# Performance work log

Measured on AMD Instinct MI355X. Metric: run time of the kernel, lower is better.

The kernel has to match this reference:

```python
import jax, jax.numpy as jnp
import numpy as np
from jax import lax

L, H, DH, D, FF = 8, 16, 64, 1024, 4096  # layers, heads, head dim, model dim, mlp hidden
B, S = 4, 512
EPS = 1e-5


def setup_inputs() -> dict:
    key = jax.random.key(0)
    ks = jax.random.split(key, 8)
    std = 0.02
    return {
        "x": jax.random.normal(ks[0], (B, S, D), jnp.float32),
        "ln1_w": jnp.ones((L, D), jnp.float32),
        "ln1_b": jnp.zeros((L, D), jnp.float32),
        "qw": jax.random.normal(ks[1], (L, H, DH, DH), jnp.float32) * std,
        "qb": jnp.zeros((L, H, DH), jnp.float32),
        "kw": jax.random.normal(ks[2], (L, H, DH, DH), jnp.float32) * std,
        "kb": jnp.zeros((L, H, DH), jnp.float32),
        "vw": jax.random.normal(ks[3], (L, H, DH, DH), jnp.float32) * std,
        "vb": jnp.zeros((L, H, DH), jnp.float32),
        "ln2_w": jnp.ones((L, D), jnp.float32),
        "ln2_b": jnp.zeros((L, D), jnp.float32),
        "w1": jax.random.normal(ks[4], (L, D, FF), jnp.float32) * std,
        "b1": jnp.zeros((L, FF), jnp.float32),
        "w2": jax.random.normal(ks[5], (L, FF, D), jnp.float32) * std,
        "b2": jnp.zeros((L, D), jnp.float32),
    }


def _layernorm(x, w, b):
    m = jnp.mean(x, axis=-1, keepdims=True)
    v = jnp.mean(jnp.square(x - m), axis=-1, keepdims=True)
    return (x - m) * lax.rsqrt(v + EPS) * w + b


def reference(x, ln1_w, ln1_b, qw, qb, kw, kb, vw, vb, ln2_w, ln2_b, w1, b1, w2, b2):
    b, s, d = x.shape
    scale = 1.0 / jnp.sqrt(jnp.asarray(DH, x.dtype))

    def layer(h, p):
        (l1w, l1b, Qw, Qb, Kw, Kb, Vw, Vb, l2w, l2b, W1, B1, W2, B2) = p
        y = _layernorm(h, l1w, l1b)
        yh = y.reshape(b, s, H, DH)
        # nn.Linear per head: y @ W.T + b, W is [out=e, in=d]
        q = jnp.einsum('bshd,hed->bshe', yh, Qw) + Qb
        k = jnp.einsum('bshd,hed->bshe', yh, Kw) + Kb
        v = jnp.einsum('bshd,hed->bshe', yh, Vw) + Vb
        attn = jax.nn.softmax(jnp.einsum('bshe,bthe->bhst', q, k) * scale, axis=-1)
        o = jnp.einsum('bhst,bthe->bshe', attn, v).reshape(b, s, d)
        h = h + o
        z = _layernorm(h, l2w, l2b)
        z = jax.nn.gelu(z @ W1 + B1, approximate=False) @ W2 + B2
        return h + z, None

    params = (ln1_w, ln1_b, qw, qb, kw, kb, vw, vb, ln2_w, ln2_b, w1, b1, w2, b2)
    out, _ = lax.scan(layer, x, params)
    return out
```

## Files before the change

kernel.cpp:

```cpp
#include <hip/hip_runtime.h>
#include <hip/hip_bf16.h>

typedef __hip_bfloat16 bf16;
typedef __bf16 bf16x8 __attribute__((ext_vector_type(8)));
typedef float f32x4 __attribute__((ext_vector_type(4)));
typedef unsigned short u16;
typedef unsigned int u32;

#define SEQ 512
#define DMODEL 1024
#define FFDIM 4096
#define NHEAD 16
#define HDIM 64
#define NB 4
#define NLAYER 8

__device__ __forceinline__ u16 f2bu(float f) {
    union { bf16 h; u16 u; } c; c.h = __float2bfloat16(f); return c.u;
}

__device__ __forceinline__ void gload16(const bf16* g, bf16* l) {
    __builtin_amdgcn_global_load_lds(
        (const __attribute__((address_space(1))) unsigned int*)g,
        (__attribute__((address_space(3))) unsigned int*)l,
        16, 0, 0);
}

template<int BM, int BN, int BK, int WM, int WN>
__device__ __forceinline__ void gemm_core(
    const bf16* __restrict__ A, int lda,
    const bf16* __restrict__ B, int ldb,
    int K,
    f32x4 (&acc)[WM/16][WN/16],
    bf16* lA, bf16* lB)
{
    constexpr int NFM = WM / 16, NFN = WN / 16;
    constexpr int WC = BN / WN;
    const int tid  = threadIdx.x;
    const int lane = tid & 63, wave = tid >> 6;
    const int wr = wave / WC, wc = wave % WC;
    const int l15 = lane & 15, l4 = lane >> 4;

    constexpr int ITA = (BM * BK) / (256 * 8);
    constexpr int ITB = (BN * BK) / (256 * 8);

    for (int kt = 0; kt < K; kt += BK) {
        __syncthreads();
#pragma unroll
        for (int it = 0; it < ITA; ++it) {
            const int f = (it * 256 + tid) * 8;
            const int r = f / BK, c = f % BK;
            gload16(A + (long)r * lda + kt + c, lA + f);
        }
#pragma unroll
        for (int it = 0; it < ITB; ++it) {
            const int f = (it * 256 + tid) * 8;
            const int r = f / BK, c = f % BK;
            gload16(B + (long)r * ldb + kt + c, lB + f);
        }
        __syncthreads();
#pragma unroll
        for (int ks = 0; ks < BK / 32; ++ks) {
            bf16x8 af[NFM], bfr[NFN];
#pragma unroll
            for (int fm = 0; fm < NFM; ++fm)
                af[fm] = *(const bf16x8*)(lA + (wr * WM + fm * 16 + l15) * BK + ks * 32 + l4 * 8);
#pragma unroll
            for (int fn = 0; fn < NFN; ++fn)
                bfr[fn] = *(const bf16x8*)(lB + (wc * WN + fn * 16 + l15) * BK + ks * 32 + l4 * 8);
#pragma unroll
            for (int fm = 0; fm < NFM; ++fm)
#pragma unroll
                for (int fn = 0; fn < NFN; ++fn)
                    acc[fm][fn] = __builtin_amdgcn_mfma_f32_16x16x32_bf16(
                        af[fm], bfr[fn], acc[fm][fn], 0, 0, 0);
        }
    }
}

__global__ __launch_bounds__(256) void k_ln(const float* __restrict__ h,
                                            const float* __restrict__ w,
                                            const float* __restrict__ bp,
                                            bf16* __restrict__ out)
{
    const int row = blockIdx.x;
    const int tid = threadIdx.x;
    const float4 x = ((const float4*)(h + (long)row * DMODEL))[tid];
    float s  = x.x + x.y + x.z + x.w;
    float s2 = x.x * x.x + x.y * x.y + x.z * x.z + x.w * x.w;
#pragma unroll
    for (int off = 32; off; off >>= 1) { s += __shfl_xor(s, off); s2 += __shfl_xor(s2, off); }
    __shared__ float rs[4], rs2[4];
    const int wave = tid >> 6;
    if ((tid & 63) == 0) { rs[wave] = s; rs2[wave] = s2; }
    __syncthreads();
    const float S1 = rs[0] + rs[1] + rs[2] + rs[3];
    const float S2 = rs2[0] + rs2[1] + rs2[2] + rs2[3];
    const float mean = S1 * (1.0f / DMODEL);
    const float var  = S2 * (1.0f / DMODEL) - mean * mean;
    const float rstd = rsqrtf(var + 1e-5f);
    const float4 wv = ((const float4*)w)[tid];
    const float4 bv = ((const float4*)bp)[tid];
    uint2 o;
    o.x = (u32)f2bu((x.x - mean) * rstd * wv.x + bv.x) |
          ((u32)f2bu((x.y - mean) * rstd * wv.y + bv.y) << 16);
    o.y = (u32)f2bu((x.z - mean) * rstd * wv.z + bv.z) |
          ((u32)f2bu((x.w - mean) * rstd * wv.w + bv.w) << 16);
    ((uint2*)(out + (long)row * DMODEL))[tid] = o;
}

__global__ __launch_bounds__(256) void k_transw(const float* __restrict__ w1,
                                                const float* __restrict__ w2,
                                                bf16* __restrict__ w1t,
                                                bf16* __restrict__ w2t)
{
    __shared__ float t[64][65];
    int bid = blockIdx.x;
    const float* src; bf16* dst; int R, C, rb, cb;
    if (bid < 1024) {
        src = w1; dst = w1t; R = DMODEL; C = FFDIM;
        rb = (bid >> 6) << 6; cb = (bid & 63) << 6;
    } else {
        bid -= 1024;
        src = w2; dst = w2t; R = FFDIM; C = DMODEL;
        rb = (bid >> 4) << 6; cb = (bid & 15) << 6;
    }
    const int tid = threadIdx.x;
#pragma unroll
    for (int i = 0; i < 16; ++i) {
        int flat = i * 256 + tid;
        int r = flat >> 6, c = flat & 63;
        t[r][c] = src[(long)(rb + r) * C + cb + c];
    }
    __syncthreads();
#pragma unroll
    for (int i = 0; i < 16; ++i) {
        int flat = i * 256 + tid;
        int c = flat >> 6, r = flat & 63;
        dst[(long)(cb + c) * R + rb + r] = __float2bfloat16(t[r][c]);
    }
}

__global__ __launch_bounds__(256) void k_qkv2(const bf16* __restrict__ y,
                                              const float* __restrict__ qwl,
                                              const float* __restrict__ kwl,
                                              const float* __restrict__ vwl,
                                              const float* __restrict__ qb,
                                              const float* __restrict__ kb,
                                              const float* __restrict__ vb,
                                              bf16* __restrict__ qh,
                                              bf16* __restrict__ kh,
                                              bf16* __restrict__ vt)
{
    __shared__ __align__(16) char lmem[128 * 64 * 2 + 64 * 64 * 2];
    bf16* lA = (bf16*)lmem;
    char* lBb = lmem + 128 * 64 * 2;

    const int tid = threadIdx.x;
    const int lane = tid & 63, wave = tid >> 6;
    const int l15 = lane & 15, l4 = lane >> 4;
    const int z = blockIdx.y;
    const int b = z >> 4, hd = z & 15;
    const bf16* A = y + (long)b * SEQ * DMODEL + hd * HDIM + (long)blockIdx.x * 128 * DMODEL;

#pragma unroll
    for (int it = 0; it < 4; ++it) {
        const int f = (it * 256 + tid) * 8;
        const int r = f >> 6, c = f & 63;
        gload16(A + (long)r * DMODEL + c, lA + f);
    }
    __syncthreads();

    bf16x8 qa[2][2];
#pragma unroll
    for (int fm = 0; fm < 2; ++fm)
#pragma unroll
        for (int ks = 0; ks < 2; ++ks)
            qa[fm][ks] = *(const bf16x8*)(lA + (wave * 32 + fm * 16 + l15) * 64 + ks * 32 + l4 * 8);

    for (int t = 0; t < 3; ++t) {
        __syncthreads();
        const float* Bsrc = ((t == 0) ? qwl : (t == 1) ? kwl : vwl) + (long)hd * HDIM * HDIM;
#pragma unroll
        for (int it = 0; it < 4; ++it) {
            const int f = (it * 256 + tid) * 4;
            const float4 v = *(const float4*)(Bsrc + f);
            uint2 o;
            o.x = (u32)f2bu(v.x) | ((u32)f2bu(v.y) << 16);
            o.y = (u32)f2bu(v.z) | ((u32)f2bu(v.w) << 16);
            const int row = f >> 6;
            const int byte = (f << 1) ^ ((row & 7) << 4);
            *(uint2*)(lBb + byte) = o;
        }
        __syncthreads();

        bf16x8 bfr[4][2];
#pragma unroll
        for (int fn = 0; fn < 4; ++fn)
#pragma unroll
            for (int ks = 0; ks < 2; ++ks) {
                const int row = fn * 16 + l15;
                int byte = (row << 7) + ((ks * 32 + l4 * 8) << 1);
                byte ^= (row & 7) << 4;
                bfr[fn][ks] = *(const bf16x8*)(lBb + byte);
            }
        f32x4 acc[2][4] = {};
#pragma unroll
        for (int ks = 0; ks < 2; ++ks)
#pragma unroll
            for (int fm = 0; fm < 2; ++fm)
#pragma unroll
                for (int fn = 0; fn < 4; ++fn)
                    acc[fm][fn] = __builtin_amdgcn_mfma_f32_16x16x32_bf16(
                        qa[fm][ks], bfr[fn][ks], acc[fm][fn], 0, 0, 0);

        const float* bias = (t == 0) ? qb : (t == 1) ? kb : vb;
#pragma unroll
        for (int fm = 0; fm < 2; ++fm)
#pragma unroll
            for (int fn = 0; fn < 4; ++fn)
#pragma unroll
                for (int r = 0; r < 4; ++r) {
                    const int srow = blockIdx.x * 128 + wave * 32 + fm * 16 + l4 * 4 + r;
                    const int e = fn * 16 + l15;
                    float v = acc[fm][fn][r] + bias[hd * HDIM + e];
                    if (t == 0) {
                        qh[((long)z * SEQ + srow) * HDIM + e] = __float2bfloat16(v * 0.125f);
                    } else if (t == 1) {
                        kh[((long)z * SEQ + srow) * HDIM + e] = __float2bfloat16(v);
                    } else {
                        vt[((long)z * HDIM + e) * SEQ + srow] = __float2bfloat16(v);
                    }
                }
    }
}

__global__ __launch_bounds__(256) void k_flash(const bf16* __restrict__ qh,
                                               const bf16* __restrict__ kh,
                                               const bf16* __restrict__ vt,
                                               float* __restrict__ h)
{
    __shared__ __align__(16) char lmem[24576];
    bf16* lQ = (bf16*)lmem;
    char* lKb = lmem + 8192;
    char* lVb = lmem + 16384;

    const int tid = threadIdx.x;
    const int lane = tid & 63, wave = tid >> 6;
    const int l15 = lane & 15, l4 = lane >> 4;
    const int z = blockIdx.y;
    const int b = z >> 4, hd = z & 15;
    const int q0 = blockIdx.x * 64;

    const bf16* Qsrc = qh + ((long)z * SEQ + q0) * HDIM;
#pragma unroll
    for (int it = 0; it < 2; ++it) {
        const int f = (it * 256 + tid) * 8;
        gload16(Qsrc + f, lQ + f);
    }
    __syncthreads();

    bf16x8 qa[2];
#pragma unroll
    for (int ks = 0; ks < 2; ++ks)
        qa[ks] = *(const bf16x8*)(lQ + (wave * 16 + l15) * 64 + ks * 32 + l4 * 8);

    char* lPb = lmem + wave * 2048;

    f32x4 O[4] = {};
    float mrun[4], lrun[4];
#pragma unroll
    for (int r = 0; r < 4; ++r) { mrun[r] = -1e30f; lrun[r] = 0.0f; }

    for (int kv = 0; kv < SEQ / 64; ++kv) {
        __syncthreads();
        const bf16* Ksrc = kh + ((long)z * SEQ + kv * 64) * HDIM;
#pragma unroll
        for (int it = 0; it < 2; ++it) {
            const int f = (it * 256 + tid) * 8;
            const int r = f >> 6;
            const uint4 v = *(const uint4*)(Ksrc + f);
            *(uint4*)(lKb + ((f << 1) ^ ((r & 7) << 4))) = v;
        }
        const bf16* Vsrc = vt + (long)z * HDIM * SEQ + kv * 64;
#pragma unroll
        for (int it = 0; it < 2; ++it) {
            const int f = (it * 256 + tid) * 8;
            const int r = f >> 6, c = f & 63;
            const uint4 v = *(const uint4*)(Vsrc + (long)r * SEQ + c);
            *(uint4*)(lVb + ((f << 1) ^ ((r & 7) << 4))) = v;
        }
        __syncthreads();

        f32x4 sa[4];
#pragma unroll
        for (int fn = 0; fn < 4; ++fn) sa[fn] = (f32x4){0.f, 0.f, 0.f, 0.f};
#pragma unroll
        for (int ks = 0; ks < 2; ++ks)
#pragma unroll
            for (int fn = 0; fn < 4; ++fn) {
                const int row = fn * 16 + l15;
                int byte = (row << 7) + ((ks * 32 + l4 * 8) << 1);
                byte ^= (row & 7) << 4;
                const bf16x8 kb_ = *(const bf16x8*)(lKb + byte);
                sa[fn] = __builtin_amdgcn_mfma_f32_16x16x32_bf16(qa[ks], kb_, sa[fn], 0, 0, 0);
            }

#pragma unroll
        for (int r = 0; r < 4; ++r) {
            float mx = fmaxf(fmaxf(sa[0][r], sa[1][r]), fmaxf(sa[2][r], sa[3][r]));
#pragma unroll
            for (int m_ = 1; m_ < 16; m_ <<= 1) mx = fmaxf(mx, __shfl_xor(mx, m_));
            const float nm = fmaxf(mrun[r], mx);
            const float al = __expf(mrun[r] - nm);
            mrun[r] = nm;
            float p0 = __expf(sa[0][r] - nm), p1 = __expf(sa[1][r] - nm);
            float p2 = __expf(sa[2][r] - nm), p3 = __expf(sa[3][r] - nm);
            float ps = p0 + p1 + p2 + p3;
#pragma unroll
            for (int m_ = 1; m_ < 16; m_ <<= 1) ps += __shfl_xor(ps, m_);
            lrun[r] = lrun[r] * al + ps;
#pragma unroll
            for (int fn = 0; fn < 4; ++fn) O[fn][r] *= al;
            const int row = l4 * 4 + r;
            const int rsw = (row & 7) << 4;
            const int rb = row << 7;
            *(u16*)(lPb + ((rb + ((0 * 16 + l15) << 1)) ^ rsw)) = f2bu(p0);
            *(u16*)(lPb + ((rb + ((1 * 16 + l15) << 1)) ^ rsw)) = f2bu(p1);
            *(u16*)(lPb + ((rb + ((2 * 16 + l15) << 1)) ^ rsw)) = f2bu(p2);
            *(u16*)(lPb + ((rb + ((3 * 16 + l15) << 1)) ^ rsw)) = f2bu(p3);
        }

#pragma unroll
        for (int ks = 0; ks < 2; ++ks) {
            const int rowp = l15;
            int pbyte = (rowp << 7) + ((ks * 32 + l4 * 8) << 1);
            pbyte ^= (rowp & 7) << 4;
            const bf16x8 pa = *(const bf16x8*)(lPb + pbyte);
#pragma unroll
            for (int fn = 0; fn < 4; ++fn) {
                const int row = fn * 16 + l15;
                int byte = (row << 7) + ((ks * 32 + l4 * 8) << 1);
                byte ^= (row & 7) << 4;
                const bf16x8 vb_ = *(const bf16x8*)(lVb + byte);
                O[fn] = __builtin_amdgcn_mfma_f32_16x16x32_bf16(pa, vb_, O[fn], 0, 0, 0);
            }
        }
    }

    float rinv[4];
#pragma unroll
    for (int r = 0; r < 4; ++r) rinv[r] = 1.0f / lrun[r];
#pragma unroll
    for (int fn = 0; fn < 4; ++fn)
#pragma unroll
        for (int r = 0; r < 4; ++r) {
            const int srow = q0 + wave * 16 + l4 * 4 + r;
            const int e = fn * 16 + l15;
            h[((long)b * SEQ + srow) * DMODEL + hd * HDIM + e] += O[fn][r] * rinv[r];
        }
}

__global__ __launch_bounds__(256) void k_gemm1(const bf16* __restrict__ zb,
                                               const bf16* __restrict__ w1t,
                                               const float* __restrict__ b1,
                                               bf16* __restrict__ ff1)
{
    constexpr int BM = 128, BN = 128, BK = 64, WM = 64, WN = 64;
    __shared__ __align__(16) bf16 lA[BM * BK];
    __shared__ __align__(16) bf16 lB[BN * BK];
    const bf16* A = zb + (long)blockIdx.x * BM * DMODEL;
    const bf16* B = w1t + (long)blockIdx.y * BN * DMODEL;
    f32x4 acc[4][4] = {};
    gemm_core<BM, BN, BK, WM, WN>(A, DMODEL, B, DMODEL, DMODEL, acc, lA, lB);

    const int lane = threadIdx.x & 63, wave = threadIdx.x >> 6;
    const int wr = wave >> 1, wc = wave & 1, l15 = lane & 15, l4 = lane >> 4;
#pragma unroll
    for (int fm = 0; fm < 4; ++fm)
#pragma unroll
        for (int fn = 0; fn < 4; ++fn)
#pragma unroll
            for (int r = 0; r < 4; ++r) {
                const int row = blockIdx.x * BM + wr * WM + fm * 16 + l4 * 4 + r;
                const int col = blockIdx.y * BN + wc * WN + fn * 16 + l15;
                const float x = acc[fm][fn][r] + b1[col];
                const float g = 0.5f * x * (1.0f + erff(x * 0.70710678118f));
                ff1[(long)row * FFDIM + col] = __float2bfloat16(g);
            }
}

__global__ __launch_bounds__(256) void k_gemm2(const bf16* __restrict__ ff1,
                                               const bf16* __restrict__ w2t,
                                               float* __restrict__ part)
{
    constexpr int BM = 128, BN = 128, BK = 64, WM = 64, WN = 64;
    constexpr int KSPLIT = FFDIM / 4;
    __shared__ __align__(16) bf16 lA[BM * BK];
    __shared__ __align__(16) bf16 lB[BN * BK];
    const int sk = blockIdx.z;
    const bf16* A = ff1 + (long)blockIdx.x * BM * FFDIM + (long)sk * KSPLIT;
    const bf16* B = w2t + (long)blockIdx.y * BN * FFDIM + (long)sk * KSPLIT;
    f32x4 acc[4][4] = {};
    gemm_core<BM, BN, BK, WM, WN>(A, FFDIM, B, FFDIM, KSPLIT, acc, lA, lB);

    float* out = part + (long)sk * (NB * SEQ) * DMODEL;
    const int lane = threadIdx.x & 63, wave = threadIdx.x >> 6;
    const int wr = wave >> 1, wc = wave & 1, l15 = lane & 15, l4 = lane >> 4;
#pragma unroll
    for (int fm = 0; fm < 4; ++fm)
#pragma unroll
        for (int fn = 0; fn < 4; ++fn)
#pragma unroll
            for (int r = 0; r < 4; ++r) {
                const int row = blockIdx.x * BM + wr * WM + fm * 16 + l4 * 4 + r;
                const int col = blockIdx.y * BN + wc * WN + fn * 16 + l15;
                out[(long)row * DMODEL + col] = acc[fm][fn][r];
            }
}

__global__ __launch_bounds__(256) void k_red2ln(const float* __restrict__ part,
                                                const float* __restrict__ b2,
                                                float* __restrict__ h,
                                                const float* __restrict__ lnw,
                                                const float* __restrict__ lnb,
                                                bf16* __restrict__ y,
                                                int do_ln)
{
    constexpr long NELT = (long)NB * SEQ * DMODEL / 4;
    const long row = blockIdx.x;
    const int tid = threadIdx.x;
    const long i = row * (DMODEL / 4) + tid;
    float4 s = ((const float4*)part)[i];
    const float4 s1 = ((const float4*)part)[i + NELT];
    const float4 s2 = ((const float4*)part)[i + 2 * NELT];
    const float4 s3 = ((const float4*)part)[i + 3 * NELT];
    const float4 bv = ((const float4*)b2)[tid];
    float4 hv = ((float4*)h)[i];
    hv.x += s.x + s1.x + s2.x + s3.x + bv.x;
    hv.y += s.y + s1.y + s2.y + s3.y + bv.y;
    hv.z += s.z + s1.z + s2.z + s3.z + bv.z;
    hv.w += s.w + s1.w + s2.w + s3.w + bv.w;
    ((float4*)h)[i] = hv;

    if (!do_ln) return;
    float ss  = hv.x + hv.y + hv.z + hv.w;
    float ss2 = hv.x * hv.x + hv.y * hv.y + hv.z * hv.z + hv.w * hv.w;
#pragma unroll
    for (int off = 32; off; off >>= 1) { ss += __shfl_xor(ss, off); ss2 += __shfl_xor(ss2, off); }
    __shared__ float rs[4], rs2[4];
    const int wave = tid >> 6;
    if ((tid & 63) == 0) { rs[wave] = ss; rs2[wave] = ss2; }
    __syncthreads();
    const float S1 = rs[0] + rs[1] + rs[2] + rs[3];
    const float S2 = rs2[0] + rs2[1] + rs2[2] + rs2[3];
    const float mean = S1 * (1.0f / DMODEL);
    const float var  = S2 * (1.0f / DMODEL) - mean * mean;
    const float rstd = rsqrtf(var + 1e-5f);
    const float4 wv = ((const float4*)lnw)[tid];
    const float4 lb = ((const float4*)lnb)[tid];
    uint2 o;
    o.x = (u32)f2bu((hv.x - mean) * rstd * wv.x + lb.x) |
          ((u32)f2bu((hv.y - mean) * rstd * wv.y + lb.y) << 16);
    o.y = (u32)f2bu((hv.z - mean) * rstd * wv.z + lb.z) |
          ((u32)f2bu((hv.w - mean) * rstd * wv.w + lb.w) << 16);
    ((uint2*)(y + row * DMODEL))[tid] = o;
}

extern "C" void kernel_launch(void* const* d_in, const int* in_sizes, int n_in,
                              void* d_out, int out_size, void* d_ws, size_t ws_size,
                              hipStream_t stream)
{
    const float* x    = (const float*)d_in[0];
    const float* ln1w = (const float*)d_in[1];
    const float* ln1b = (const float*)d_in[2];
    const float* qw   = (const float*)d_in[3];
    const float* qb   = (const float*)d_in[4];
    const float* kw   = (const float*)d_in[5];
    const float* kb   = (const float*)d_in[6];
    const float* vw   = (const float*)d_in[7];
    const float* vb   = (const float*)d_in[8];
    const float* ln2w = (const float*)d_in[9];
    const float* ln2b = (const float*)d_in[10];
    const float* w1   = (const float*)d_in[11];
    const float* b1   = (const float*)d_in[12];
    const float* w2   = (const float*)d_in[13];
    const float* b2   = (const float*)d_in[14];

    char* ws = (char*)d_ws;
    const size_t MB = 1024 * 1024;
    bf16* y    = (bf16*)(ws + 0 * MB);
    bf16* zb   = (bf16*)(ws + 4 * MB);
    bf16* qh   = (bf16*)(ws + 8 * MB);
    bf16* kh   = (bf16*)(ws + 12 * MB);
    bf16* vt   = (bf16*)(ws + 16 * MB);
    bf16* ff1  = (bf16*)(ws + 20 * MB);
    bf16* w1t  = (bf16*)(ws + 36 * MB);
    bf16* w2t  = (bf16*)(ws + 44 * MB);
    float* part = (float*)(ws + 53 * MB);

    float* h = (float*)d_out;
    hipMemcpyAsync(d_out, x, (size_t)NB * SEQ * DMODEL * sizeof(float),
                   hipMemcpyDeviceToDevice, stream);

    k_ln<<<NB * SEQ, 256, 0, stream>>>(h, ln1w, ln1b, y);

    for (int l = 0; l < NLAYER; ++l) {
        k_qkv2<<<dim3(4, NB * NHEAD), 256, 0, stream>>>(
            y, qw + (long)l * 65536, kw + (long)l * 65536, vw + (long)l * 65536,
            qb + l * NHEAD * HDIM, kb + l * NHEAD * HDIM, vb + l * NHEAD * HDIM,
            qh, kh, vt);
        k_flash<<<dim3(SEQ / 64, NB * NHEAD), 256, 0, stream>>>(qh, kh, vt, h);
        k_ln<<<NB * SEQ, 256, 0, stream>>>(h, ln2w + l * DMODEL, ln2b + l * DMODEL, zb);
        k_transw<<<2048, 256, 0, stream>>>(w1 + (long)l * DMODEL * FFDIM,
                                           w2 + (long)l * DMODEL * FFDIM, w1t, w2t);
        k_gemm1<<<dim3(16, 32), 256, 0, stream>>>(zb, w1t, b1 + l * FFDIM, ff1);
        k_gemm2<<<dim3(16, 8, 4), 256, 0, stream>>>(ff1, w2t, part);
        const int last = (l == NLAYER - 1);
        k_red2ln<<<NB * SEQ, 256, 0, stream>>>(part, b2 + l * DMODEL, h,
                                               ln1w + (l + 1) * DMODEL * (1 - last),
                                               ln1b + (l + 1) * DMODEL * (1 - last),
                                               y, !last);
    }
}
```

Baseline: 1.008 ms.

## Double-buffer MLP GEMMs with swizzled LDS, 256x128 tiles, vectorize weight transpose

Replaces the synchronous single-buffer GEMM core with a two-stage LDS pipeline: the global-to-LDS load for tile t+2 overlaps MFMA on tile t, using vmcnt waits and raw barriers. It also XOR-swizzles the LDS layout to reduce bank conflicts and moves to 512-thread blocks with 256x128 tiles, which raises per-block reuse but halves the grid. The weight transpose kernel now uses float4 loads and packed bf16 stores. Risks include the 96KB LDS limiting occupancy, fewer blocks per GEMM, and fragile hand-written waitcnt logic.

```diff
diff --git a/kernel.cpp b/kernel.cpp
--- a/kernel.cpp
+++ b/kernel.cpp
@@ -15,6 +15,8 @@
 #define NB 4
 #define NLAYER 8
 
+#define SBAR() asm volatile("s_barrier" ::: "memory")
+
 __device__ __forceinline__ u16 f2bu(float f) {
     union { bf16 h; u16 u; } c; c.h = __float2bfloat16(f); return c.u;
 }
@@ -26,55 +28,93 @@
         16, 0, 0);
 }
 
-template<int BM, int BN, int BK, int WM, int WN>
-__device__ __forceinline__ void gemm_core(
+__device__ __forceinline__ void gemm_pipe(
     const bf16* __restrict__ A, int lda,
     const bf16* __restrict__ B, int ldb,
-    int K,
-    f32x4 (&acc)[WM/16][WN/16],
-    bf16* lA, bf16* lB)
-{
-    constexpr int NFM = WM / 16, NFN = WN / 16;
-    constexpr int WC = BN / WN;
-    const int tid  = threadIdx.x;
-    const int lane = tid & 63, wave = tid >> 6;
-    const int wr = wave / WC, wc = wave % WC;
+    int nkt,
+    f32x4 (&acc)[8][2],
+    char* lA, char* lB)
+{
+    const int tid = threadIdx.x;
+    const int lane = tid & 63;
+    const int wave = tid >> 6;
+    const int wr = wave >> 2, wc = wave & 3;
     const int l15 = lane & 15, l4 = lane >> 4;
 
-    constexpr int ITA = (BM * BK) / (256 * 8);
-    constexpr int ITB = (BN * BK) / (256 * 8);
-
-    for (int kt = 0; kt < K; kt += BK) {
-        __syncthreads();
-#pragma unroll
-        for (int it = 0; it < ITA; ++it) {
-            const int f = (it * 256 + tid) * 8;
-            const int r = f / BK, c = f % BK;
-            gload16(A + (long)r * lda + kt + c, lA + f);
-        }
-#pragma unroll
-        for (int it = 0; it < ITB; ++it) {
-            const int f = (it * 256 + tid) * 8;
-            const int r = f / BK, c = f % BK;
-            gload16(B + (long)r * ldb + kt + c, lB + f);
-        }
-        __syncthreads();
-#pragma unroll
-        for (int ks = 0; ks < BK / 32; ++ks) {
-            bf16x8 af[NFM], bfr[NFN];
-#pragma unroll
-            for (int fm = 0; fm < NFM; ++fm)
-                af[fm] = *(const bf16x8*)(lA + (wr * WM + fm * 16 + l15) * BK + ks * 32 + l4 * 8);
-#pragma unroll
-            for (int fn = 0; fn < NFN; ++fn)
-                bfr[fn] = *(const bf16x8*)(lB + (wc * WN + fn * 16 + l15) * BK + ks * 32 + l4 * 8);
-#pragma unroll
-            for (int fm = 0; fm < NFM; ++fm)
-#pragma unroll
-                for (int fn = 0; fn < NFN; ++fn)
-                    acc[fm][fn] = __builtin_amdgcn_mfma_f32_16x16x32_bf16(
-                        af[fm], bfr[fn], acc[fm][fn], 0, 0, 0);
-        }
+    auto stage = [&](int c, int t) {
+        const bf16* Ak = A + t * 64;
+        const bf16* Bk = B + t * 64;
+        bf16* dA = (bf16*)(lA + c * 32768);
+        bf16* dB = (bf16*)(lB + c * 16384);
+#pragma unroll
+        for (int it = 0; it < 4; ++it) {
+            const int e = (it * 512 + tid) * 8;
+            const int r = e >> 6;
+            const int cb = (e & 63) * 2;
+            const int sc = (cb ^ (((r >> 2) & 1) << 5)) >> 1;
+            gload16(Ak + (long)r * lda + sc, dA + e);
+        }
+#pragma unroll
+        for (int it = 0; it < 2; ++it) {
+            const int e = (it * 512 + tid) * 8;
+            const int r = e >> 6;
+            const int cb = (e & 63) * 2;
+            const int sc = (cb ^ (((r >> 2) & 1) << 5)) >> 1;
+            gload16(Bk + (long)r * ldb + sc, dB + e);
+        }
+    };
+
+    stage(0, 0);
+    stage(1, 1);
+    asm volatile("s_waitcnt vmcnt(6)" ::: "memory");
+    SBAR();
+
+    for (int t = 0; t < nkt; ++t) {
+        const int cur = t & 1;
+        const char* bA = lA + cur * 32768;
+        const char* bB = lB + cur * 16384;
+
+        bf16x8 bf_[2][2];
+#pragma unroll
+        for (int fn = 0; fn < 2; ++fn)
+#pragma unroll
+            for (int ks = 0; ks < 2; ++ks) {
+                const int row = wc * 32 + fn * 16 + l15;
+                int byte = row * 128 + (ks * 32 + l4 * 8) * 2;
+                byte ^= ((row >> 2) & 1) << 5;
+                bf_[fn][ks] = *(const bf16x8*)(bB + byte);
+            }
+#pragma unroll
+        for (int q = 0; q < 4; ++q) {
+            bf16x8 af[2][2];
+#pragma unroll
+            for (int i = 0; i < 2; ++i)
+#pragma unroll
+                for (int ks = 0; ks < 2; ++ks) {
+                    const int row = wr * 128 + (q * 2 + i) * 16 + l15;
+                    int byte = row * 128 + (ks * 32 + l4 * 8) * 2;
+                    byte ^= ((row >> 2) & 1) << 5;
+                    af[i][ks] = *(const bf16x8*)(bA + byte);
+                }
+            __builtin_amdgcn_s_setprio(1);
+#pragma unroll
+            for (int i = 0; i < 2; ++i)
+#pragma unroll
+                for (int fn = 0; fn < 2; ++fn)
+#pragma unroll
+                    for (int ks = 0; ks < 2; ++ks)
+                        acc[q * 2 + i][fn] = __builtin_amdgcn_mfma_f32_16x16x32_bf16(
+                            af[i][ks], bf_[fn][ks], acc[q * 2 + i][fn], 0, 0, 0);
+            __builtin_amdgcn_s_setprio(0);
+        }
+        SBAR();
+        if (t + 2 < nkt) {
+            stage(cur, t + 2);
+            asm volatile("s_waitcnt vmcnt(6)" ::: "memory");
+        } else {
+            asm volatile("s_waitcnt vmcnt(0)" ::: "memory");
+        }
+        SBAR();
     }
 }
 
@@ -126,18 +166,22 @@
         rb = (bid >> 4) << 6; cb = (bid & 15) << 6;
     }
     const int tid = threadIdx.x;
-#pragma unroll
-    for (int i = 0; i < 16; ++i) {
-        int flat = i * 256 + tid;
-        int r = flat >> 6, c = flat & 63;
-        t[r][c] = src[(long)(rb + r) * C + cb + c];
+    const int lr = tid >> 4;
+    const int lc = (tid & 15) * 4;
+#pragma unroll
+    for (int i = 0; i < 4; ++i) {
+        const int r = i * 16 + lr;
+        const float4 v = *(const float4*)(src + (long)(rb + r) * C + cb + lc);
+        t[r][lc] = v.x; t[r][lc + 1] = v.y; t[r][lc + 2] = v.z; t[r][lc + 3] = v.w;
     }
     __syncthreads();
 #pragma unroll
-    for (int i = 0; i < 16; ++i) {
-        int flat = i * 256 + tid;
-        int c = flat >> 6, r = flat & 63;
-        dst[(long)(cb + c) * R + rb + r] = __float2bfloat16(t[r][c]);
+    for (int i = 0; i < 4; ++i) {
+        const int c = i * 16 + lr;
+        uint2 o;
+        o.x = (u32)f2bu(t[lc][c])     | ((u32)f2bu(t[lc + 1][c]) << 16);
+        o.y = (u32)f2bu(t[lc + 2][c]) | ((u32)f2bu(t[lc + 3][c]) << 16);
+        *(uint2*)(dst + (long)(cb + c) * R + rb + lc) = o;
     }
 }
 
@@ -361,60 +405,57 @@
         }
 }
 
-__global__ __launch_bounds__(256) void k_gemm1(const bf16* __restrict__ zb,
-                                               const bf16* __restrict__ w1t,
-                                               const float* __restrict__ b1,
-                                               bf16* __restrict__ ff1)
-{
-    constexpr int BM = 128, BN = 128, BK = 64, WM = 64, WN = 64;
-    __shared__ __align__(16) bf16 lA[BM * BK];
-    __shared__ __align__(16) bf16 lB[BN * BK];
-    const bf16* A = zb + (long)blockIdx.x * BM * DMODEL;
-    const bf16* B = w1t + (long)blockIdx.y * BN * DMODEL;
-    f32x4 acc[4][4] = {};
-    gemm_core<BM, BN, BK, WM, WN>(A, DMODEL, B, DMODEL, DMODEL, acc, lA, lB);
+__global__ __launch_bounds__(512, 2) void k_gemm1(const bf16* __restrict__ zb,
+                                                  const bf16* __restrict__ w1t,
+                                                  const float* __restrict__ b1,
+                                                  bf16* __restrict__ ff1)
+{
+    __shared__ __align__(16) char lmem[98304];
+    const bf16* A = zb + (long)blockIdx.x * 256 * DMODEL;
+    const bf16* B = w1t + (long)blockIdx.y * 128 * DMODEL;
+    f32x4 acc[8][2] = {};
+    gemm_pipe(A, DMODEL, B, DMODEL, DMODEL / 64, acc, lmem, lmem + 65536);
 
     const int lane = threadIdx.x & 63, wave = threadIdx.x >> 6;
-    const int wr = wave >> 1, wc = wave & 1, l15 = lane & 15, l4 = lane >> 4;
-#pragma unroll
-    for (int fm = 0; fm < 4; ++fm)
-#pragma unroll
-        for (int fn = 0; fn < 4; ++fn)
+    const int wr = wave >> 2, wc = wave & 3;
+    const int l15 = lane & 15, l4 = lane >> 4;
+#pragma unroll
+    for (int fm = 0; fm < 8; ++fm)
+#pragma unroll
+        for (int fn = 0; fn < 2; ++fn)
 #pragma unroll
             for (int r = 0; r < 4; ++r) {
-                const int row = blockIdx.x * BM + wr * WM + fm * 16 + l4 * 4 + r;
-                const int col = blockIdx.y * BN + wc * WN + fn * 16 + l15;
+                const int row = blockIdx.x * 256 + wr * 128 + fm * 16 + l4 * 4 + r;
+                const int col = blockIdx.y * 128 + wc * 32 + fn * 16 + l15;
                 const float x = acc[fm][fn][r] + b1[col];
                 const float g = 0.5f * x * (1.0f + erff(x * 0.70710678118f));
                 ff1[(long)row * FFDIM + col] = __float2bfloat16(g);
             }
 }
 
-__global__ __launch_bounds__(256) void k_gemm2(const bf16* __restrict__ ff1,
-                                               const bf16* __restrict__ w2t,
-                                               float* __restrict__ part)
-{
-    constexpr int BM = 128, BN = 128, BK = 64, WM = 64, WN = 64;
-    constexpr int KSPLIT = FFDIM / 4;
-    __shared__ __align__(16) bf16 lA[BM * BK];
-    __shared__ __align__(16) bf16 lB[BN * BK];
+__global__ __launch_bounds__(512, 2) void k_gemm2(const bf16* __restrict__ ff1,
+                                                  const bf16* __restrict__ w2t,
+                                                  float* __restrict__ part)
+{
+    __shared__ __align__(16) char lmem[98304];
     const int sk = blockIdx.z;
-    const bf16* A = ff1 + (long)blockIdx.x * BM * FFDIM + (long)sk * KSPLIT;
-    const bf16* B = w2t + (long)blockIdx.y * BN * FFDIM + (long)sk * KSPLIT;
-    f32x4 acc[4][4] = {};
-    gemm_core<BM, BN, BK, WM, WN>(A, FFDIM, B, FFDIM, KSPLIT, acc, lA, lB);
+    const bf16* A = ff1 + (long)blockIdx.x * 256 * FFDIM + (long)sk * 1024;
+    const bf16* B = w2t + (long)blockIdx.y * 128 * FFDIM + (long)sk * 1024;
+    f32x4 acc[8][2] = {};
+    gemm_pipe(A, FFDIM, B, FFDIM, 1024 / 64, acc, lmem, lmem + 65536);
 
     float* out = part + (long)sk * (NB * SEQ) * DMODEL;
     const int lane = threadIdx.x & 63, wave = threadIdx.x >> 6;
-    const int wr = wave >> 1, wc = wave & 1, l15 = lane & 15, l4 = lane >> 4;
-#pragma unroll
-    for (int fm = 0; fm < 4; ++fm)
-#pragma unroll
-        for (int fn = 0; fn < 4; ++fn)
+    const int wr = wave >> 2, wc = wave & 3;
+    const int l15 = lane & 15, l4 = lane >> 4;
+#pragma unroll
+    for (int fm = 0; fm < 8; ++fm)
+#pragma unroll
+        for (int fn = 0; fn < 2; ++fn)
 #pragma unroll
             for (int r = 0; r < 4; ++r) {
-                const int row = blockIdx.x * BM + wr * WM + fm * 16 + l4 * 4 + r;
-                const int col = blockIdx.y * BN + wc * WN + fn * 16 + l15;
+                const int row = blockIdx.x * 256 + wr * 128 + fm * 16 + l4 * 4 + r;
+                const int col = blockIdx.y * 128 + wc * 32 + fn * 16 + l15;
                 out[(long)row * DMODEL + col] = acc[fm][fn][r];
             }
 }
@@ -514,8 +555,8 @@
         k_ln<<<NB * SEQ, 256, 0, stream>>>(h, ln2w + l * DMODEL, ln2b + l * DMODEL, zb);
         k_transw<<<2048, 256, 0, stream>>>(w1 + (long)l * DMODEL * FFDIM,
                                            w2 + (long)l * DMODEL * FFDIM, w1t, w2t);
-        k_gemm1<<<dim3(16, 32), 256, 0, stream>>>(zb, w1t, b1 + l * FFDIM, ff1);
-        k_gemm2<<<dim3(16, 8, 4), 256, 0, stream>>>(ff1, w2t, part);
+        k_gemm1<<<dim3(8, 32), 512, 0, stream>>>(zb, w1t, b1 + l * FFDIM, ff1);
+        k_gemm2<<<dim3(8, 8, 4), 512, 0, stream>>>(ff1, w2t, part);
         const int last = (l == NLAYER - 1);
         k_red2ln<<<NB * SEQ, 256, 0, stream>>>(part, b2 + l * DMODEL, h,
                                                ln1w + (l + 1) * DMODEL * (1 - last),
```

Result: faster. 955.2 us (-5.3%).
